# Kernel optimization log

Measured on AMD Instinct MI355X. Metric: run time of the kernel, lower is better.

## Reference

```python
import jax, jax.numpy as jnp
import numpy as np

N_HEAD = 16
N_KV_HEAD = 4


def setup_inputs() -> dict:
    key = jax.random.key(0)
    ks = jax.random.split(key, 5)
    B, T, C = 2, 2048, 2048
    kv_dim = (C // N_HEAD) * N_KV_HEAD  # 512
    s = 0.02
    return {
        "x": jax.random.normal(ks[0], (B, T, C), dtype=jnp.float32),
        "Wq": jax.random.normal(ks[1], (C, C), dtype=jnp.float32) * s,
        "Wk": jax.random.normal(ks[2], (kv_dim, C), dtype=jnp.float32) * s,
        "Wv": jax.random.normal(ks[3], (kv_dim, C), dtype=jnp.float32) * s,
        "Wo": jax.random.normal(ks[4], (C, C), dtype=jnp.float32) * s,
    }


def reference(x, Wq, Wk, Wv, Wo):
    B, T, C = x.shape
    H, KV = N_HEAD, N_KV_HEAD
    hd = C // H          # 128
    g = H // KV          # query groups per kv head
    scale = hd ** -0.5

    # projections (torch Linear: y = x @ W.T)
    # q heads laid out so head h -> (kv = h // g, group j = h % g),
    # matching repeat_interleave(groups, dim=1) on k/v.
    q = (x @ Wq.T).reshape(B, T, KV, g, hd).transpose(0, 2, 3, 1, 4)  # [B,KV,g,T,hd]
    k = (x @ Wk.T).reshape(B, T, KV, hd).transpose(0, 2, 1, 3)        # [B,KV,T,hd]
    v = (x @ Wv.T).reshape(B, T, KV, hd).transpose(0, 2, 1, 3)        # [B,KV,T,hd]

    # GQA attention without materializing repeated KV heads
    att = jnp.einsum("bkgtd,bksd->bkgts", q, k) * scale  # [B,KV,g,T,T]
    causal = jnp.tril(jnp.ones((T, T), dtype=bool))
    att = jnp.where(causal, att, jnp.float32(-jnp.inf))
    att = jax.nn.softmax(att, axis=-1)
    # dropout p = config.dropout assumed 0 (eval/deterministic reference)

    out = jnp.einsum("bkgts,bksd->bkgtd", att, v)          # [B,KV,g,T,hd]
    out = out.transpose(0, 3, 1, 2, 4).reshape(B, T, C)    # [B,T,C]
    return out @ Wo.T
```

## Files before the change

kernel.cpp:

```cpp
#include <hip/hip_runtime.h>
#include <hip/hip_bf16.h>
#include <math.h>

typedef __bf16 bf16;
typedef __bf16 bf16x4 __attribute__((ext_vector_type(4)));
typedef __bf16 bf16x8 __attribute__((ext_vector_type(8)));
typedef float f32x4 __attribute__((ext_vector_type(4)));
typedef float f32x16 __attribute__((ext_vector_type(16)));
typedef unsigned int uint32x4 __attribute__((ext_vector_type(4)));

__device__ __forceinline__ void gload_lds16(const void* g, void* l) {
  __builtin_amdgcn_global_load_lds(
      (const __attribute__((address_space(1))) void*)g,
      (__attribute__((address_space(3))) void*)l, 16, 0, 0);
}

__device__ __forceinline__ unsigned int packbf(float a, float b) {
  union { bf16 h[2]; unsigned int u; } x;
  x.h[0] = (bf16)a; x.h[1] = (bf16)b;
  return x.u;
}

__global__ void cvt_all(const float* __restrict__ x,  const float* __restrict__ Wq,
                        const float* __restrict__ Wk, const float* __restrict__ Wv,
                        const float* __restrict__ Wo,
                        bf16* __restrict__ xb, bf16* __restrict__ wqkv, bf16* __restrict__ wob,
                        float qscale) {
  const int stride = gridDim.x * blockDim.x;
  const int total4 = 4718592;
  for (int i = blockIdx.x * blockDim.x + threadIdx.x; i < total4; i += stride) {
    const size_t e = (size_t)i * 4;
    const float* src; bf16* dst; size_t off; float sc = 1.f;
    if (e < 8388608)       { src = x;  dst = xb;            off = e; }
    else if (e < 12582912) { src = Wq; dst = wqkv;          off = e - 8388608; sc = qscale; }
    else if (e < 13631488) { src = Wk; dst = wqkv + 4194304; off = e - 12582912; }
    else if (e < 14680064) { src = Wv; dst = wqkv + 5242880; off = e - 13631488; }
    else                   { src = Wo; dst = wob;           off = e - 14680064; }
    float4 v = *(const float4*)(src + off);
    bf16x4 o;
    o[0] = (bf16)(v.x * sc); o[1] = (bf16)(v.y * sc);
    o[2] = (bf16)(v.z * sc); o[3] = (bf16)(v.w * sc);
    *(bf16x4*)(dst + off) = o;
  }
}

template <int MODE>
__global__ __launch_bounds__(512, 1)
void gemm256(const bf16* __restrict__ A, const bf16* __restrict__ B,
             float* __restrict__ Cf, bf16* __restrict__ Qb, bf16* __restrict__ Kb,
             bf16* __restrict__ Vtb, int K, int Nst) {
  __shared__ __align__(16) char sA[65536];
  __shared__ __align__(16) char sB[65536];

  const int tid  = threadIdx.x;
  const int lane = tid & 63, w = tid >> 6;
  const int wr   = w >> 2, wc = w & 3;
  const int fr   = lane & 15, fq = lane >> 4;
  const int brow = blockIdx.y, bcol = blockIdx.x;

  f32x4 acc[8][4] = {};

  const bf16* Ab = A + (size_t)brow * 256 * K;
  const bf16* Bb = B + (size_t)bcol * 256 * K;
  const int NT = K >> 6;

  auto stage_half = [&](int tau, int hh) {
    const bf16* src = (hh < 2) ? Ab : Bb;
    char* dst = ((hh < 2) ? sA : sB) + (tau & 1) * 32768 + (hh & 1) * 16384;
#pragma unroll
    for (int i = 0; i < 2; ++i) {
      const int ci = i * 512 + tid, r = ci >> 3, ck = ci & 7;
      gload_lds16(src + (size_t)((hh & 1) * 128 + r) * K + tau * 64 + ((ck ^ (r & 7)) * 8),
                  dst + i * 8192 + w * 1024);
    }
  };

  stage_half(0, 0); stage_half(0, 1); stage_half(0, 2); stage_half(0, 3);
  stage_half(1, 2); stage_half(1, 3);
  asm volatile("s_waitcnt vmcnt(4)" ::: "memory");
  __builtin_amdgcn_s_barrier();

  for (int t = 0; t < NT; ++t) {
    const char* pAh = sA + (t & 1) * 32768 + wr * 16384;
    const char* pBh = sB + (t & 1) * 32768 + (wc >> 1) * 16384;
    bf16x8 bfr[4][2];
#pragma unroll
    for (int ph = 0; ph < 4; ++ph) {
      bf16x8 af[2][2];
#pragma unroll
      for (int mi = 0; mi < 2; ++mi) {
        const int r = (2 * ph + mi) * 16 + fr;
#pragma unroll
        for (int ks = 0; ks < 2; ++ks)
          af[mi][ks] = *(const bf16x8*)(pAh + r * 128 + (((ks * 4 + fq) ^ (r & 7)) * 16));
      }
      if (ph == 0) {
#pragma unroll
        for (int ni = 0; ni < 4; ++ni) {
          const int r = (wc & 1) * 64 + ni * 16 + fr;
#pragma unroll
          for (int ks = 0; ks < 2; ++ks)
            bfr[ni][ks] = *(const bf16x8*)(pBh + r * 128 + (((ks * 4 + fq) ^ (r & 7)) * 16));
        }
      }
      if (ph == 0 && t + 1 < NT) stage_half(t + 1, 0);
      if (ph == 1 && t + 1 < NT) stage_half(t + 1, 1);
      if (ph == 2 && t + 2 < NT) stage_half(t + 2, 2);
      if (ph == 3 && t + 2 < NT) stage_half(t + 2, 3);
      if (ph == 0) asm volatile("s_waitcnt lgkmcnt(8)" ::: "memory");
      __builtin_amdgcn_s_barrier();
      asm volatile("s_waitcnt lgkmcnt(0)" ::: "memory");
      __builtin_amdgcn_sched_barrier(0);
      __builtin_amdgcn_s_setprio(1);
#pragma unroll
      for (int mi = 0; mi < 2; ++mi)
#pragma unroll
        for (int ni = 0; ni < 4; ++ni)
#pragma unroll
          for (int ks = 0; ks < 2; ++ks)
            acc[2 * ph + mi][ni] =
                __builtin_amdgcn_mfma_f32_16x16x32_bf16(af[mi][ks], bfr[ni][ks], acc[2 * ph + mi][ni], 0, 0, 0);
      __builtin_amdgcn_s_setprio(0);
      if (ph == 3) {
        if (t == NT - 2) asm volatile("s_waitcnt vmcnt(0)" ::: "memory");
        else if (t < NT - 2) asm volatile("s_waitcnt vmcnt(4)" ::: "memory");
      }
      __builtin_amdgcn_s_barrier();
    }
  }

  const int r0 = brow * 256 + wr * 128 + fq * 4;
  const int c0 = bcol * 256 + wc * 64 + fr;
#pragma unroll
  for (int mi = 0; mi < 8; ++mi)
#pragma unroll
    for (int ni = 0; ni < 4; ++ni)
#pragma unroll
      for (int j = 0; j < 4; ++j) {
        const int r = r0 + mi * 16 + j;
        const int c = c0 + ni * 16;
        const float v = acc[mi][ni][j];
        if constexpr (MODE == 0) {
          Cf[(size_t)r * Nst + c] = v;
        } else {
          if (c < 2048)       Qb[(size_t)r * 2048 + c] = (bf16)v;
          else if (c < 2560)  Kb[(size_t)r * 512 + (c - 2048)] = (bf16)v;
          else                Vtb[(size_t)(c - 2560) * 4096 + r] = (bf16)v;
        }
      }
}

__global__ __launch_bounds__(256, 2)
void attn_fwd(const bf16* __restrict__ Q, const bf16* __restrict__ Kg_,
              const bf16* __restrict__ Vt, bf16* __restrict__ AO) {
  const int T = 2048, C = 2048, KVD = 512, MTOK = 4096;
  const int bid = blockIdx.x;
  const int qt  = (bid < 256) ? (15 - (bid >> 5)) : ((bid >> 5) - 8);
  const int sub = bid & 31;
  const int h = sub & 15, b = sub >> 4;
  const int kvh = h >> 2;
  const int lane = threadIdx.x & 63, w = threadIdx.x >> 6;
  const int hi = lane >> 5, lo = lane & 31;

  __shared__ __align__(16) char smem[65536];
  char* sK  = smem;
  char* sVt = smem + 32768;

  const bf16* Qg = Q   + (size_t)b * T * C + (size_t)h * 128;
  const bf16* Kg = Kg_ + (size_t)b * T * KVD + (size_t)kvh * 128;
  const bf16* Vg = Vt  + (size_t)kvh * 128 * MTOK + (size_t)b * T;

  const int q0 = qt * 128;
  const int qw = q0 + w * 32;

  bf16x8 qf[8];
#pragma unroll
  for (int ks = 0; ks < 8; ++ks)
    qf[ks] = *(const bf16x8*)(Qg + (size_t)(qw + lo) * C + ks * 16 + hi * 8);

  f32x16 ot[4] = {};
  float mstat = -INFINITY, lstat = 0.f;

  const int nt = 2 * qt + 2;

  auto stage = [&](int t, int buf) {
#pragma unroll
    for (int i = 0; i < 4; ++i) {
      const int ci = i * 256 + threadIdx.x;
      const int rk = ci >> 4, ck = ci & 15;
      gload_lds16(Kg + (size_t)(t * 64 + rk) * KVD + ((ck ^ (rk & 7)) * 8),
                  sK + buf * 16384 + i * 4096 + w * 1024);
      const int rv = ci >> 3, cv = ci & 7;
      gload_lds16(Vg + (size_t)rv * MTOK + t * 64 + ((cv ^ (rv & 7)) * 8),
                  sVt + buf * 16384 + i * 4096 + w * 1024);
    }
  };

  auto compute = [&](int t, int buf) {
    const int kv0 = t * 64;
    if (kv0 > qw + 31) return;
    const char* kb = sK + buf * 16384;
    const char* vb = sVt + buf * 16384;

    f32x16 sa[2] = {};
    __builtin_amdgcn_s_setprio(1);
#pragma unroll
    for (int ks = 0; ks < 8; ++ks) {
#pragma unroll
      for (int nb = 0; nb < 2; ++nb) {
        const int r = nb * 32 + lo;
        bf16x8 kf = *(const bf16x8*)(kb + (r * 256 + (((ks * 2 + hi) ^ (r & 7)) * 16)));
        sa[nb] = __builtin_amdgcn_mfma_f32_32x32x16_bf16(kf, qf[ks], sa[nb], 0, 0, 0);
      }
    }
    __builtin_amdgcn_s_setprio(0);
    if (kv0 + 63 > qw) {
      const int qg = qw + lo;
#pragma unroll
      for (int nb = 0; nb < 2; ++nb)
#pragma unroll
        for (int r = 0; r < 16; ++r) {
          const int kvg = kv0 + nb * 32 + (r & 3) + 8 * (r >> 2) + 4 * hi;
          if (kvg > qg) sa[nb][r] = -1e30f;
        }
    }
    float pm = -INFINITY;
#pragma unroll
    for (int nb = 0; nb < 2; ++nb)
#pragma unroll
      for (int r = 0; r < 16; ++r) pm = fmaxf(pm, sa[nb][r]);
    pm = fmaxf(pm, __shfl_xor(pm, 32));

    if (__any(pm > mstat + 8.f)) {
      const float mn = fmaxf(mstat, pm);
      const float rs = __expf(mstat - mn);
      mstat = mn;
      lstat *= rs;
#pragma unroll
      for (int db = 0; db < 4; ++db)
#pragma unroll
        for (int r = 0; r < 16; ++r) ot[db][r] *= rs;
    }

    float ls = 0.f;
    unsigned int pw[2][8];
#pragma unroll
    for (int nb = 0; nb < 2; ++nb)
#pragma unroll
      for (int j = 0; j < 8; ++j) {
        const float e0 = __expf(sa[nb][2 * j]     - mstat);
        const float e1 = __expf(sa[nb][2 * j + 1] - mstat);
        ls += e0 + e1;
        pw[nb][j] = packbf(e0, e1);
      }
    ls += __shfl_xor(ls, 32);
    lstat += ls;

#pragma unroll
    for (int nb = 0; nb < 2; ++nb) {
      unsigned int pj[8];
#pragma unroll
      for (int j = 0; j < 8; ++j) pj[j] = __shfl_xor(pw[nb][j], 32);
      __builtin_amdgcn_s_setprio(1);
#pragma unroll
      for (int half = 0; half < 2; ++half) {
        const int x = half * 4;
        uint32x4 bw;
        bw[0] = hi ? pj[x + 2] : pw[nb][x + 0];
        bw[1] = hi ? pj[x + 3] : pw[nb][x + 1];
        bw[2] = hi ? pw[nb][x + 2] : pj[x + 0];
        bw[3] = hi ? pw[nb][x + 3] : pj[x + 1];
        const bf16x8 pb = __builtin_bit_cast(bf16x8, bw);
        const int ks = nb * 2 + half;
#pragma unroll
        for (int db = 0; db < 4; ++db) {
          const int rv = db * 32 + lo;
          bf16x8 vf = *(const bf16x8*)(vb + (rv * 128 + (((ks * 2 + hi) ^ (rv & 7)) * 16)));
          ot[db] = __builtin_amdgcn_mfma_f32_32x32x16_bf16(vf, pb, ot[db], 0, 0, 0);
        }
      }
      __builtin_amdgcn_s_setprio(0);
    }
  };

  stage(0, 0);
  for (int t = 0; t < nt - 1; ++t) {
    stage(t + 1, (t + 1) & 1);
    asm volatile("s_waitcnt vmcnt(8)" ::: "memory");
    __builtin_amdgcn_s_barrier();
    compute(t, t & 1);
    __builtin_amdgcn_s_barrier();
  }
  asm volatile("s_waitcnt vmcnt(0)" ::: "memory");
  __builtin_amdgcn_s_barrier();
  compute(nt - 1, (nt - 1) & 1);

  __syncthreads();
  char* sO = smem;
  const float inv = 1.f / lstat;
  const int lq = w * 32 + lo;
#pragma unroll
  for (int db = 0; db < 4; ++db) {
#pragma unroll
    for (int j = 0; j < 8; ++j) {
      const int r = 2 * j;
      const int d = db * 32 + (r & 3) + 8 * (r >> 2) + 4 * hi;
      const unsigned int pv = packbf(ot[db][r] * inv, ot[db][r + 1] * inv);
      *(unsigned int*)(sO + (lq * 256 + ((2 * d) ^ (16 * (lq & 7))))) = pv;
    }
  }
  __syncthreads();
  bf16* Og = AO + (size_t)b * T * C + (size_t)h * 128;
#pragma unroll
  for (int i = 0; i < 8; ++i) {
    const int cid = i * 256 + threadIdx.x;
    const int rq = cid >> 4, c = cid & 15;
    bf16x8 vv = *(const bf16x8*)(sO + (rq * 256 + ((c * 16) ^ (16 * (rq & 7)))));
    *(bf16x8*)(Og + (size_t)(q0 + rq) * C + c * 8) = vv;
  }
}

extern "C" void kernel_launch(void* const* d_in, const int* in_sizes, int n_in,
                              void* d_out, int out_size, void* d_ws, size_t ws_size,
                              hipStream_t stream) {
  const float* x  = (const float*)d_in[0];
  const float* Wq = (const float*)d_in[1];
  const float* Wk = (const float*)d_in[2];
  const float* Wv = (const float*)d_in[3];
  const float* Wo = (const float*)d_in[4];
  float* out = (float*)d_out;

  char* ws = (char*)d_ws;
  bf16* xb   = (bf16*)(ws);
  bf16* wqkv = (bf16*)(ws + 16777216);
  bf16* wob  = (bf16*)(ws + 29360128);
  bf16* Qb   = (bf16*)(ws + 37748736);
  bf16* Kb   = (bf16*)(ws + 54525952);
  bf16* Vtb  = (bf16*)(ws + 58720256);
  bf16* AOb  = (bf16*)(ws + 62914560);

  const float scale = 0.08838834764831845f;
  cvt_all<<<2048, 256, 0, stream>>>(x, Wq, Wk, Wv, Wo, xb, wqkv, wob, scale);

  gemm256<1><<<dim3(12, 16), 512, 0, stream>>>(xb, wqkv, nullptr, Qb, Kb, Vtb, 2048, 0);

  attn_fwd<<<512, 256, 0, stream>>>(Qb, Kb, Vtb, AOb);

  gemm256<0><<<dim3(8, 16), 512, 0, stream>>>(AOb, wob, out, nullptr, nullptr, nullptr, 2048, 2048);
}
```

Measured before the change: 227.3 us.

## Replace 256x256 GEMM with 128x128 tiles, triple-buffered LDS and XCD-aware block remap

Swaps the 512-thread 256x256-tile GEMM for a 256-thread 128x128-tile kernel with K-step 32, a three-stage LDS ring buffer, and a block-index swizzle that spreads consecutive tiles across the 8 XCDs. The aim is more workgroups (768/512 instead of 192/128) to fill the 256 CUs and to raise occupancy with smaller LDS use. In exchange each tile gets less data reuse, the LDS layout loses the XOR swizzle (possible bank conflicts), and there are more barriers per unit of K.

Result: slower. 276.0 us (+21.4%).

```diff
diff --git a/kernel.cpp b/kernel.cpp
--- a/kernel.cpp
+++ b/kernel.cpp
@@ -45,94 +45,74 @@
 }
 
 template <int MODE>
-__global__ __launch_bounds__(512, 1)
-void gemm256(const bf16* __restrict__ A, const bf16* __restrict__ B,
+__global__ __launch_bounds__(256)
+void gemm128(const bf16* __restrict__ A, const bf16* __restrict__ B,
              float* __restrict__ Cf, bf16* __restrict__ Qb, bf16* __restrict__ Kb,
-             bf16* __restrict__ Vtb, int K, int Nst) {
-  __shared__ __align__(16) char sA[65536];
-  __shared__ __align__(16) char sB[65536];
+             bf16* __restrict__ Vtb, int K, int gridN, int Nst) {
+  __shared__ __align__(16) char smem[49152];
 
   const int tid  = threadIdx.x;
   const int lane = tid & 63, w = tid >> 6;
-  const int wr   = w >> 2, wc = w & 3;
+  const int wr   = w >> 1, wc = w & 1;
   const int fr   = lane & 15, fq = lane >> 4;
-  const int brow = blockIdx.y, bcol = blockIdx.x;
-
-  f32x4 acc[8][4] = {};
-
-  const bf16* Ab = A + (size_t)brow * 256 * K;
-  const bf16* Bb = B + (size_t)bcol * 256 * K;
-  const int NT = K >> 6;
-
-  auto stage_half = [&](int tau, int hh) {
-    const bf16* src = (hh < 2) ? Ab : Bb;
-    char* dst = ((hh < 2) ? sA : sB) + (tau & 1) * 32768 + (hh & 1) * 16384;
+
+  const int nwg = gridDim.x;
+  const int wg  = (blockIdx.x & 7) * (nwg >> 3) + (blockIdx.x >> 3);
+  const int brow = wg / gridN, bcol = wg % gridN;
+
+  f32x4 acc[4][4] = {};
+
+  const bf16* Ab = A + (size_t)brow * 128 * K;
+  const bf16* Bb = B + (size_t)bcol * 128 * K;
+  const int NT = K >> 5;
+
+  auto stage = [&](int t, int buf) {
+    char* base = smem + buf * 16384;
 #pragma unroll
     for (int i = 0; i < 2; ++i) {
-      const int ci = i * 512 + tid, r = ci >> 3, ck = ci & 7;
-      gload_lds16(src + (size_t)((hh & 1) * 128 + r) * K + tau * 64 + ((ck ^ (r & 7)) * 8),
-                  dst + i * 8192 + w * 1024);
+      const int ci = i * 256 + tid;
+      const int kc = ci >> 7, row = ci & 127;
+      gload_lds16(Ab + (size_t)row * K + t * 32 + kc * 8, base + i * 4096 + w * 1024);
+      gload_lds16(Bb + (size_t)row * K + t * 32 + kc * 8, base + 8192 + i * 4096 + w * 1024);
     }
   };
 
-  stage_half(0, 0); stage_half(0, 1); stage_half(0, 2); stage_half(0, 3);
-  stage_half(1, 2); stage_half(1, 3);
-  asm volatile("s_waitcnt vmcnt(4)" ::: "memory");
-  __builtin_amdgcn_s_barrier();
-
+  stage(0, 0);
+  stage(1, 1);
   for (int t = 0; t < NT; ++t) {
-    const char* pAh = sA + (t & 1) * 32768 + wr * 16384;
-    const char* pBh = sB + (t & 1) * 32768 + (wc >> 1) * 16384;
-    bf16x8 bfr[4][2];
-#pragma unroll
-    for (int ph = 0; ph < 4; ++ph) {
-      bf16x8 af[2][2];
-#pragma unroll
-      for (int mi = 0; mi < 2; ++mi) {
-        const int r = (2 * ph + mi) * 16 + fr;
-#pragma unroll
-        for (int ks = 0; ks < 2; ++ks)
-          af[mi][ks] = *(const bf16x8*)(pAh + r * 128 + (((ks * 4 + fq) ^ (r & 7)) * 16));
-      }
-      if (ph == 0) {
-#pragma unroll
-        for (int ni = 0; ni < 4; ++ni) {
-          const int r = (wc & 1) * 64 + ni * 16 + fr;
-#pragma unroll
-          for (int ks = 0; ks < 2; ++ks)
-            bfr[ni][ks] = *(const bf16x8*)(pBh + r * 128 + (((ks * 4 + fq) ^ (r & 7)) * 16));
-        }
-      }
-      if (ph == 0 && t + 1 < NT) stage_half(t + 1, 0);
-      if (ph == 1 && t + 1 < NT) stage_half(t + 1, 1);
-      if (ph == 2 && t + 2 < NT) stage_half(t + 2, 2);
-      if (ph == 3 && t + 2 < NT) stage_half(t + 2, 3);
-      if (ph == 0) asm volatile("s_waitcnt lgkmcnt(8)" ::: "memory");
-      __builtin_amdgcn_s_barrier();
-      asm volatile("s_waitcnt lgkmcnt(0)" ::: "memory");
-      __builtin_amdgcn_sched_barrier(0);
-      __builtin_amdgcn_s_setprio(1);
-#pragma unroll
-      for (int mi = 0; mi < 2; ++mi)
-#pragma unroll
-        for (int ni = 0; ni < 4; ++ni)
-#pragma unroll
-          for (int ks = 0; ks < 2; ++ks)
-            acc[2 * ph + mi][ni] =
-                __builtin_amdgcn_mfma_f32_16x16x32_bf16(af[mi][ks], bfr[ni][ks], acc[2 * ph + mi][ni], 0, 0, 0);
-      __builtin_amdgcn_s_setprio(0);
-      if (ph == 3) {
-        if (t == NT - 2) asm volatile("s_waitcnt vmcnt(0)" ::: "memory");
-        else if (t < NT - 2) asm volatile("s_waitcnt vmcnt(4)" ::: "memory");
-      }
-      __builtin_amdgcn_s_barrier();
-    }
-  }
-
-  const int r0 = brow * 256 + wr * 128 + fq * 4;
-  const int c0 = bcol * 256 + wc * 64 + fr;
-#pragma unroll
-  for (int mi = 0; mi < 8; ++mi)
+    const int buf = t % 3;
+    if (t + 2 < NT) {
+      stage(t + 2, (t + 2) % 3);
+      asm volatile("s_waitcnt vmcnt(8)" ::: "memory");
+    } else if (t + 2 == NT) {
+      asm volatile("s_waitcnt vmcnt(4)" ::: "memory");
+    } else {
+      asm volatile("s_waitcnt vmcnt(0)" ::: "memory");
+    }
+    __builtin_amdgcn_s_barrier();
+
+    const char* pA = smem + buf * 16384;
+    const char* pB = pA + 8192;
+    bf16x8 af[4], bfr[4];
+#pragma unroll
+    for (int i = 0; i < 4; ++i) {
+      af[i]  = *(const bf16x8*)(pA + fq * 2048 + (wr * 64 + i * 16 + fr) * 16);
+      bfr[i] = *(const bf16x8*)(pB + fq * 2048 + (wc * 64 + i * 16 + fr) * 16);
+    }
+    __builtin_amdgcn_s_setprio(1);
+#pragma unroll
+    for (int mi = 0; mi < 4; ++mi)
+#pragma unroll
+      for (int ni = 0; ni < 4; ++ni)
+        acc[mi][ni] = __builtin_amdgcn_mfma_f32_16x16x32_bf16(af[mi], bfr[ni], acc[mi][ni], 0, 0, 0);
+    __builtin_amdgcn_s_setprio(0);
+    __builtin_amdgcn_s_barrier();
+  }
+
+  const int r0 = brow * 128 + wr * 64 + fq * 4;
+  const int c0 = bcol * 128 + wc * 64 + fr;
+#pragma unroll
+  for (int mi = 0; mi < 4; ++mi)
 #pragma unroll
     for (int ni = 0; ni < 4; ++ni)
 #pragma unroll
@@ -342,9 +322,9 @@
   const float scale = 0.08838834764831845f;
   cvt_all<<<2048, 256, 0, stream>>>(x, Wq, Wk, Wv, Wo, xb, wqkv, wob, scale);
 
-  gemm256<1><<<dim3(12, 16), 512, 0, stream>>>(xb, wqkv, nullptr, Qb, Kb, Vtb, 2048, 0);
+  gemm128<1><<<768, 256, 0, stream>>>(xb, wqkv, nullptr, Qb, Kb, Vtb, 2048, 24, 0);
 
   attn_fwd<<<512, 256, 0, stream>>>(Qb, Kb, Vtb, AOb);
 
-  gemm256<0><<<dim3(8, 16), 512, 0, stream>>>(AOb, wob, out, nullptr, nullptr, nullptr, 2048, 2048);
-}
+  gemm128<0><<<512, 256, 0, stream>>>(AOb, wob, out, nullptr, nullptr, nullptr, 2048, 16, 2048);
+}
```
